# Kernel tuning notes

Measured on AMD Instinct MI355X. Metric: run time of the kernel, lower is better.

The kernel has to match this reference:

```python
import jax, jax.numpy as jnp
import numpy as np

EPS = 1e-12  # guard sqrt(0) for numerical safety


def setup_inputs() -> dict:
    key = jax.random.key(0)
    k1, k2 = jax.random.split(key)
    N, P, D = 500000, 256, 128
    embeddings = jax.random.normal(k1, (N, D), dtype=jnp.float32)
    # prototypes initialized like torch.rand (uniform [0,1))
    prototypes = jax.random.uniform(k2, (P, D), dtype=jnp.float32)
    return {"embeddings": embeddings, "prototypes": prototypes}


def reference(embeddings, prototypes):
    # Euclidean distance via the cdist-as-GEMM identity:
    # ||e - p||^2 = ||e||^2 + ||p||^2 - 2 e.p  -> avoids (N,P,D) intermediate.
    e2 = jnp.sum(embeddings * embeddings, axis=-1, keepdims=True)  # (N,1)
    p2 = jnp.sum(prototypes * prototypes, axis=-1)[None, :]        # (1,P)
    cross = embeddings @ prototypes.T                              # (N,P)
    d2 = jnp.maximum(e2 + p2 - 2.0 * cross, EPS)
    dists = jnp.sqrt(d2)                                           # (N,P)
    # module returns -dists reshaped to (N, 1, P) for the 2D-input path
    return -dists[:, None, :]
```

## Files before the change

kernel.cpp:

```cpp
#include <hip/hip_runtime.h>
#include <hip/hip_bf16.h>

typedef __bf16 bf16x8 __attribute__((ext_vector_type(8)));
typedef float  f32x4  __attribute__((ext_vector_type(4)));

constexpr int D = 128;
constexpr int P = 256;
constexpr float EPS = 1e-12f;

__global__ __launch_bounds__(256, 3)
void proto_dist_kernel(const float* __restrict__ emb,
                       const float* __restrict__ proto,
                       float* __restrict__ out,
                       int N, int ntiles)
{
    const int lane = threadIdx.x & 63;
    const int wave = threadIdx.x >> 6;
    const int quad = lane >> 4;
    const int l15  = lane & 15;
    const int colbase = wave * 64;

    bf16x8 bfrag[4][4];
    float  p2[4];
    #pragma unroll
    for (int t = 0; t < 4; ++t) {
        const int n = colbase + t * 16 + l15;
        const float* src = proto + n * D + quad * 8;
        float s = 0.f;
        #pragma unroll
        for (int ks = 0; ks < 4; ++ks) {
            f32x4 lo = *(const f32x4*)(src + ks * 32);
            f32x4 hi = *(const f32x4*)(src + ks * 32 + 4);
            s += lo.x*lo.x + lo.y*lo.y + lo.z*lo.z + lo.w*lo.w;
            s += hi.x*hi.x + hi.y*hi.y + hi.z*hi.z + hi.w*hi.w;
            bf16x8 f;
            f[0]=(__bf16)lo.x; f[1]=(__bf16)lo.y; f[2]=(__bf16)lo.z; f[3]=(__bf16)lo.w;
            f[4]=(__bf16)hi.x; f[5]=(__bf16)hi.y; f[6]=(__bf16)hi.z; f[7]=(__bf16)hi.w;
            bfrag[t][ks] = f;
        }
        s += __shfl_xor(s, 16);
        s += __shfl_xor(s, 32);
        p2[t] = s;
    }

    f32x4 rlo[4], rhi[4];
    {
        const int row0 = blockIdx.x * 16;
        int rowA = row0 + l15;
        if (rowA > N - 1) rowA = N - 1;
        const float* arow = emb + (long)rowA * D + quad * 8;
        #pragma unroll
        for (int ks = 0; ks < 4; ++ks) {
            rlo[ks] = *(const f32x4*)(arow + ks * 32);
            rhi[ks] = *(const f32x4*)(arow + ks * 32 + 4);
        }
    }

    for (int tile = blockIdx.x; tile < ntiles; tile += gridDim.x) {
        bf16x8 afrag[4];
        float e2p = 0.f;
        #pragma unroll
        for (int ks = 0; ks < 4; ++ks) {
            f32x4 lo = rlo[ks], hi = rhi[ks];
            e2p += lo.x*lo.x + lo.y*lo.y + lo.z*lo.z + lo.w*lo.w;
            e2p += hi.x*hi.x + hi.y*hi.y + hi.z*hi.z + hi.w*hi.w;
            bf16x8 f;
            f[0]=(__bf16)lo.x; f[1]=(__bf16)lo.y; f[2]=(__bf16)lo.z; f[3]=(__bf16)lo.w;
            f[4]=(__bf16)hi.x; f[5]=(__bf16)hi.y; f[6]=(__bf16)hi.z; f[7]=(__bf16)hi.w;
            afrag[ks] = f;
        }

        const int tnext = tile + gridDim.x;
        if (tnext < ntiles) {
            const int row0n = tnext * 16;
            int rowA = row0n + l15;
            if (rowA > N - 1) rowA = N - 1;
            const float* arow = emb + (long)rowA * D + quad * 8;
            #pragma unroll
            for (int ks = 0; ks < 4; ++ks) {
                rlo[ks] = *(const f32x4*)(arow + ks * 32);
                rhi[ks] = *(const f32x4*)(arow + ks * 32 + 4);
            }
        }

        float e2full = e2p;
        e2full += __shfl_xor(e2full, 16);
        e2full += __shfl_xor(e2full, 32);

        f32x4 acc[4];
        const f32x4 zero = {0.f, 0.f, 0.f, 0.f};
        #pragma unroll
        for (int t = 0; t < 4; ++t) acc[t] = zero;
        #pragma unroll
        for (int ks = 0; ks < 4; ++ks) {
            #pragma unroll
            for (int t = 0; t < 4; ++t) {
                acc[t] = __builtin_amdgcn_mfma_f32_16x16x32_bf16(
                    afrag[ks], bfrag[t][ks], acc[t], 0, 0, 0);
            }
        }

        float e2r[4];
        #pragma unroll
        for (int r = 0; r < 4; ++r)
            e2r[r] = __shfl(e2full, quad * 4 + r);

        const int row0 = tile * 16;
        float* obase = out + (long)(row0 + quad * 4) * P + colbase + l15;

        if (row0 + 16 <= N) {
            #pragma unroll
            for (int t = 0; t < 4; ++t) {
                #pragma unroll
                for (int r = 0; r < 4; ++r) {
                    float d2 = fmaf(-2.f, acc[t][r], e2r[r] + p2[t]);
                    d2 = fmaxf(d2, EPS);
                    __builtin_nontemporal_store(-__builtin_sqrtf(d2),
                                                obase + (long)r * P + t * 16);
                }
            }
        } else {
            #pragma unroll
            for (int t = 0; t < 4; ++t) {
                #pragma unroll
                for (int r = 0; r < 4; ++r) {
                    const int grow = row0 + quad * 4 + r;
                    if (grow < N) {
                        float d2 = fmaf(-2.f, acc[t][r], e2r[r] + p2[t]);
                        d2 = fmaxf(d2, EPS);
                        __builtin_nontemporal_store(-__builtin_sqrtf(d2),
                                                    obase + (long)r * P + t * 16);
                    }
                }
            }
        }
    }
}

extern "C" void kernel_launch(void* const* d_in, const int* in_sizes, int n_in,
                              void* d_out, int out_size, void* d_ws, size_t ws_size,
                              hipStream_t stream)
{
    const float* emb   = (const float*)d_in[0];
    const float* proto = (const float*)d_in[1];
    float* out = (float*)d_out;

    const int N = in_sizes[0] / D;
    const int ntiles = (N + 15) / 16;
    int blocks = ntiles < 2048 ? ntiles : 2048;

    proto_dist_kernel<<<dim3(blocks), dim3(256), 0, stream>>>(emb, proto, out, N, ntiles);
}
```

Measured before the change: 740.7 us.

## Stage output tile through LDS for coalesced row stores; shrink grid to 768 blocks

Each wave writes its 16x64 distance tile into a padded LDS buffer, then reads it back row by row so each store covers a full 64-float contiguous row segment, replacing scattered 16-wide column stores. It also switches to the hardware sqrt intrinsic and cuts the persistent grid from 2048 to 768 blocks. The aim is better write coalescing on the output stream, which dominates the traffic. The cost is extra LDS traffic and reduced parallelism, and there is no barrier between the LDS write and read, which is safe only because each wave uses its own region.

```diff
diff --git a/kernel.cpp b/kernel.cpp
--- a/kernel.cpp
+++ b/kernel.cpp
@@ -7,6 +7,7 @@
 constexpr int D = 128;
 constexpr int P = 256;
 constexpr float EPS = 1e-12f;
+constexpr int PSTR = 66;
 
 __global__ __launch_bounds__(256, 3)
 void proto_dist_kernel(const float* __restrict__ emb,
@@ -14,11 +15,14 @@
                        float* __restrict__ out,
                        int N, int ntiles)
 {
+    __shared__ float stage[4][16 * PSTR];
+
     const int lane = threadIdx.x & 63;
     const int wave = threadIdx.x >> 6;
     const int quad = lane >> 4;
     const int l15  = lane & 15;
     const int colbase = wave * 64;
+    float* const mystage = stage[wave];
 
     bf16x8 bfrag[4][4];
     float  p2[4];
@@ -45,8 +49,7 @@
 
     f32x4 rlo[4], rhi[4];
     {
-        const int row0 = blockIdx.x * 16;
-        int rowA = row0 + l15;
+        int rowA = blockIdx.x * 16 + l15;
         if (rowA > N - 1) rowA = N - 1;
         const float* arow = emb + (long)rowA * D + quad * 8;
         #pragma unroll
@@ -72,8 +75,7 @@
 
         const int tnext = tile + gridDim.x;
         if (tnext < ntiles) {
-            const int row0n = tnext * 16;
-            int rowA = row0n + l15;
+            int rowA = tnext * 16 + l15;
             if (rowA > N - 1) rowA = N - 1;
             const float* arow = emb + (long)rowA * D + quad * 8;
             #pragma unroll
@@ -105,32 +107,32 @@
         for (int r = 0; r < 4; ++r)
             e2r[r] = __shfl(e2full, quad * 4 + r);
 
+        #pragma unroll
+        for (int t = 0; t < 4; ++t) {
+            #pragma unroll
+            for (int r = 0; r < 4; ++r) {
+                float d2 = fmaf(-2.f, acc[t][r], e2r[r] + p2[t]);
+                d2 = fmaxf(d2, EPS);
+                mystage[(quad * 4 + r) * PSTR + t * 16 + l15] =
+                    -__builtin_amdgcn_sqrtf(d2);
+            }
+        }
+
         const int row0 = tile * 16;
-        float* obase = out + (long)(row0 + quad * 4) * P + colbase + l15;
-
         if (row0 + 16 <= N) {
             #pragma unroll
-            for (int t = 0; t < 4; ++t) {
-                #pragma unroll
-                for (int r = 0; r < 4; ++r) {
-                    float d2 = fmaf(-2.f, acc[t][r], e2r[r] + p2[t]);
-                    d2 = fmaxf(d2, EPS);
-                    __builtin_nontemporal_store(-__builtin_sqrtf(d2),
-                                                obase + (long)r * P + t * 16);
-                }
+            for (int row = 0; row < 16; ++row) {
+                float v = mystage[row * PSTR + lane];
+                __builtin_nontemporal_store(
+                    v, out + (long)(row0 + row) * P + colbase + lane);
             }
         } else {
             #pragma unroll
-            for (int t = 0; t < 4; ++t) {
-                #pragma unroll
-                for (int r = 0; r < 4; ++r) {
-                    const int grow = row0 + quad * 4 + r;
-                    if (grow < N) {
-                        float d2 = fmaf(-2.f, acc[t][r], e2r[r] + p2[t]);
-                        d2 = fmaxf(d2, EPS);
-                        __builtin_nontemporal_store(-__builtin_sqrtf(d2),
-                                                    obase + (long)r * P + t * 16);
-                    }
+            for (int row = 0; row < 16; ++row) {
+                if (row0 + row < N) {
+                    float v = mystage[row * PSTR + lane];
+                    __builtin_nontemporal_store(
+                        v, out + (long)(row0 + row) * P + colbase + lane);
                 }
             }
         }
@@ -147,7 +149,7 @@
 
     const int N = in_sizes[0] / D;
     const int ntiles = (N + 15) / 16;
-    int blocks = ntiles < 2048 ? ntiles : 2048;
+    int blocks = ntiles < 768 ? ntiles : 768;
 
     proto_dist_kernel<<<dim3(blocks), dim3(256), 0, stream>>>(emb, proto, out, N, ntiles);
 }
```

New measurement: 690.9 us. 1.07x faster.
